# Performance work log

Hardware: AMD Instinct MI355X
Metric: run time of the kernel (lower is better)

## Reference

```python
import jax, jax.numpy as jnp
import numpy as np

DIM = 128
HEADS = 4
DIM_HEAD = 32
HIDDEN = HEADS * DIM_HEAD  # 128
SCALE = DIM_HEAD ** -0.5


def setup_inputs() -> dict:
    key = jax.random.key(0)
    k1, k2, k3, k4 = jax.random.split(key, 4)
    x = jax.random.normal(k1, (2, DIM, 16, 64, 64), dtype=jnp.float32)
    # conv2d 1x1 weights == channel matmuls
    Wqkv = jax.random.normal(k2, (3 * HIDDEN, DIM), dtype=jnp.float32) * (DIM ** -0.5)
    Wout = jax.random.normal(k3, (DIM, HIDDEN), dtype=jnp.float32) * (HIDDEN ** -0.5)
    bout = jax.random.normal(k4, (DIM,), dtype=jnp.float32) * 0.01
    return {"x": x, "Wqkv": Wqkv, "Wout": Wout, "bout": bout}


def reference(x, Wqkv, Wout, bout):
    b, c, f, h, w = x.shape
    n = h * w
    # 'b c f h w -> (b f) c (h w)'
    xf = jnp.transpose(x, (0, 2, 1, 3, 4)).reshape(b * f, c, n)
    # 1x1 conv == channel projection
    qkv = jnp.einsum('oc,bcn->bon', Wqkv, xf)  # (bf, 3*hidden, n)
    q, k, v = jnp.split(qkv, 3, axis=1)
    def to_heads(t):
        return t.reshape(b * f, HEADS, DIM_HEAD, n)  # 'b (h c) n -> b h c n'
    q, k, v = to_heads(q), to_heads(k), to_heads(v)
    q = jax.nn.softmax(q, axis=-2) * SCALE   # softmax over dim_head axis
    k = jax.nn.softmax(k, axis=-1)           # softmax over spatial axis
    v = v / n
    # context: (bf, h, d, e); out: (bf, h, e, n)
    context = jnp.einsum('bhdn,bhen->bhde', k, v)
    out = jnp.einsum('bhde,bhdn->bhen', context, q)
    out = out.reshape(b * f, HIDDEN, n)      # '(h c) merge'
    out = jnp.einsum('oc,bcn->bon', Wout, out) + bout[None, :, None]
    # '(b f) c (h w) -> b c f h w'
    out = out.reshape(b, f, c, h, w).transpose(0, 2, 1, 3, 4)
    return out
```

## Files before the change

### kernel.cpp

```cpp
#include <hip/hip_runtime.h>


constexpr float kSCALE = 0.17677669529663687f;

typedef __attribute__((ext_vector_type(8))) short short8;
typedef __attribute__((ext_vector_type(4))) float f32x4;

__device__ __forceinline__ float bfu2f(unsigned int u) {
  union { unsigned int i; float f; } c; c.i = u << 16; return c.f;
}
__device__ __forceinline__ unsigned short f2bf(float f) {
  union { float f; unsigned int i; } c; c.f = f;
  unsigned int r = c.i + 0x7fffu + ((c.i >> 16) & 1u);
  return (unsigned short)(r >> 16);
}
__device__ __forceinline__ void pack8(const float* v, unsigned short* dst16) {
  union { unsigned short u[8]; uint4 q; } t;
  #pragma unroll
  for (int i = 0; i < 8; ++i) t.u[i] = f2bf(v[i]);
  *(uint4*)dst16 = t.q;
}

__global__ __launch_bounds__(256) void k_wconv(const float* __restrict__ W,
                                               unsigned short* __restrict__ Wbf) {
  const int i = (blockIdx.x * 256 + threadIdx.x) * 4;
  const float4 v = *(const float4*)&W[i];
  union { unsigned short u[4]; uint2 q; } t;
  t.u[0] = f2bf(v.x); t.u[1] = f2bf(v.y); t.u[2] = f2bf(v.z); t.u[3] = f2bf(v.w);
  *(uint2*)&Wbf[i] = t.q;
}

__global__ __launch_bounds__(512, 4) void k_fqkv(const float* __restrict__ x,
                                                 const unsigned short* __restrict__ Wbf,
                                                 unsigned short* __restrict__ qsm,
                                                 float* __restrict__ ctxp,
                                                 float* __restrict__ sexp) {
  __shared__ __align__(16) unsigned short R0[64 * 128];
  __shared__ __align__(16) unsigned short EK[128 * 64];
  __shared__ __align__(16) unsigned short VV[128 * 64];
  const int ntile = blockIdx.x, fr = blockIdx.y;
  const int bb = fr >> 4, ff = fr & 15;
  const int tid = threadIdx.x;
  const float* xfr = x + ((size_t)bb * 2048 + ff) * 4096;

  {
    const int nn = tid & 63, cg = tid >> 6;
    const int ng = ntile * 64 + nn;
    #pragma unroll
    for (int p = 0; p < 2; ++p) {
      const int c8 = cg * 2 + p;
      float v[8];
      #pragma unroll
      for (int j = 0; j < 8; ++j) v[j] = xfr[(size_t)(c8 * 8 + j) * 65536 + ng];
      pack8(v, &R0[nn * 128 + ((c8 * 8) ^ ((nn & 7) << 3))]);
    }
  }
  __syncthreads();

  const int l = tid & 63, w = tid >> 6;
  const int wo = (w >> 1) * 96, wn = (w & 1) * 32;
  const int lr = l & 15, lg = l >> 4;
  f32x4 acc[6][2];
  #pragma unroll
  for (int i = 0; i < 6; ++i) { acc[i][0] = 0.f; acc[i][1] = 0.f; }

  #pragma unroll
  for (int ks = 0; ks < 4; ++ks) {
    const int k0 = ks * 32 + lg * 8;
    short8 a[6], b[2];
    #pragma unroll
    for (int i = 0; i < 6; ++i) a[i] = *(const short8*)&Wbf[(size_t)(wo + 16 * i + lr) * 128 + k0];
    #pragma unroll
    for (int j = 0; j < 2; ++j) {
      const int n = wn + 16 * j + lr;
      b[j] = *(const short8*)&R0[n * 128 + (k0 ^ ((n & 7) << 3))];
    }
    #pragma unroll
    for (int i = 0; i < 6; ++i)
      #pragma unroll
      for (int j = 0; j < 2; ++j)
        acc[i][j] = __builtin_amdgcn_mfma_f32_16x16x32_bf16(a[i], b[j], acc[i][j], 0, 0, 0);
  }

  #pragma unroll
  for (int i = 0; i < 6; ++i) {
    const int grow = wo + 16 * i;
    if (grow >= 128 && grow < 256) {
      #pragma unroll
      for (int j = 0; j < 2; ++j) {
        const int n = wn + 16 * j + lr;
        #pragma unroll
        for (int r = 0; r < 4; ++r) {
          const int dd = grow - 128 + 4 * lg + r;
          EK[dd * 64 + (n ^ ((dd & 7) << 3))] = f2bf(__expf(acc[i][j][r]));
        }
      }
    } else if (grow >= 256) {
      #pragma unroll
      for (int j = 0; j < 2; ++j) {
        const int n = wn + 16 * j + lr;
        #pragma unroll
        for (int r = 0; r < 4; ++r) {
          const int e = grow - 256 + 4 * lg + r;
          VV[e * 64 + (n ^ ((e & 7) << 3))] = f2bf(acc[i][j][r]);
        }
      }
    }
  }
  #pragma unroll
  for (int i0 = 0; i0 < 6; i0 += 2) {
    const int grow0 = wo + 16 * i0;
    if (grow0 < 128) {
      const int h = grow0 >> 5;
      #pragma unroll
      for (int j = 0; j < 2; ++j) {
        const int n = wn + 16 * j + lr;
        float v0[4], v1[4];
        float m = -1e30f;
        #pragma unroll
        for (int r = 0; r < 4; ++r) {
          v0[r] = acc[i0][j][r]; v1[r] = acc[i0 + 1][j][r];
          m = fmaxf(m, fmaxf(v0[r], v1[r]));
        }
        m = fmaxf(m, __shfl_xor(m, 16));
        m = fmaxf(m, __shfl_xor(m, 32));
        float s = 0.f;
        #pragma unroll
        for (int r = 0; r < 4; ++r) {
          v0[r] = __expf(v0[r] - m); v1[r] = __expf(v1[r] - m);
          s += v0[r] + v1[r];
        }
        s += __shfl_xor(s, 16);
        s += __shfl_xor(s, 32);
        const float inv = 1.f / s;
        union { unsigned short u[4]; uint2 q; } t0, t1;
        #pragma unroll
        for (int r = 0; r < 4; ++r) { t0.u[r] = f2bf(v0[r] * inv); t1.u[r] = f2bf(v1[r] * inv); }
        unsigned short* qb = qsm + ((size_t)fr * 4096 + ntile * 64 + n) * 128 + h * 32 + 4 * lg;
        *(uint2*)&qb[0]  = t0.q;
        *(uint2*)&qb[16] = t1.q;
      }
    }
  }
  __syncthreads();

  const int bp = fr * 64 + ntile;
  if (w < 4) {
    const int h = w;
    f32x4 c2[2][2];
    c2[0][0] = 0.f; c2[0][1] = 0.f; c2[1][0] = 0.f; c2[1][1] = 0.f;
    #pragma unroll
    for (int ks = 0; ks < 2; ++ks) {
      const int k0 = ks * 32 + lg * 8;
      short8 a2[2], b2[2];
      #pragma unroll
      for (int i2 = 0; i2 < 2; ++i2) {
        const int row = h * 32 + 16 * i2 + lr;
        a2[i2] = *(const short8*)&EK[row * 64 + (k0 ^ ((row & 7) << 3))];
      }
      #pragma unroll
      for (int j2 = 0; j2 < 2; ++j2) {
        const int row = h * 32 + 16 * j2 + lr;
        b2[j2] = *(const short8*)&VV[row * 64 + (k0 ^ ((row & 7) << 3))];
      }
      #pragma unroll
      for (int i2 = 0; i2 < 2; ++i2)
        #pragma unroll
        for (int j2 = 0; j2 < 2; ++j2)
          c2[i2][j2] = __builtin_amdgcn_mfma_f32_16x16x32_bf16(a2[i2], b2[j2], c2[i2][j2], 0, 0, 0);
    }
    float* cp = ctxp + ((size_t)bp * 4 + h) * 1024;
    #pragma unroll
    for (int i2 = 0; i2 < 2; ++i2)
      #pragma unroll
      for (int j2 = 0; j2 < 2; ++j2)
        #pragma unroll
        for (int r = 0; r < 4; ++r)
          cp[(16 * i2 + 4 * lg + r) * 32 + 16 * j2 + lr] = c2[i2][j2][r];
  } else {
    const int h = w - 4;
    const int rl = l & 31, half = l >> 5;
    const int row = h * 32 + rl;
    float s = 0.f;
    #pragma unroll
    for (int m = 0; m < 4; ++m) {
      const int ng = (half * 32 + m * 8) ^ ((row & 7) << 3);
      const uint4 u = *(const uint4*)&EK[row * 64 + ng];
      s += bfu2f(u.x & 0xffffu) + bfu2f(u.x >> 16) + bfu2f(u.y & 0xffffu) + bfu2f(u.y >> 16)
         + bfu2f(u.z & 0xffffu) + bfu2f(u.z >> 16) + bfu2f(u.w & 0xffffu) + bfu2f(u.w >> 16);
    }
    s += __shfl_xor(s, 32);
    if (half == 0) sexp[(size_t)bp * 128 + row] = s;
  }
}

__global__ __launch_bounds__(256) void k_mbuild(const float* __restrict__ Wout,
                                                const float* __restrict__ ctxp,
                                                const float* __restrict__ sexp,
                                                unsigned short* __restrict__ Mbf) {
  __shared__ float Wo[128][33];
  __shared__ float cn[32][36];
  __shared__ float ses[32];
  const int h = blockIdx.x, fr = blockIdx.y, tid = threadIdx.x;

  float4 c4 = make_float4(0.f, 0.f, 0.f, 0.f);
  {
    const float* base = ctxp + ((size_t)fr * 64) * 4096 + h * 1024 + tid * 4;
    #pragma unroll 8
    for (int p = 0; p < 64; ++p) {
      const float4 v = *(const float4*)&base[(size_t)p * 4096];
      c4.x += v.x; c4.y += v.y; c4.z += v.z; c4.w += v.w;
    }
  }
  if (tid < 32) {
    float s = 0.f;
    const float* sb = sexp + ((size_t)fr * 64) * 128 + h * 32 + tid;
    #pragma unroll 8
    for (int p = 0; p < 64; ++p) s += sb[(size_t)p * 128];
    ses[tid] = s;
  }
  {
    const int o = tid >> 1, e0 = (tid & 1) * 16;
    #pragma unroll
    for (int q = 0; q < 4; ++q) {
      const float4 v = *(const float4*)&Wout[o * 128 + h * 32 + e0 + 4 * q];
      Wo[o][e0 + 4 * q] = v.x; Wo[o][e0 + 4 * q + 1] = v.y;
      Wo[o][e0 + 4 * q + 2] = v.z; Wo[o][e0 + 4 * q + 3] = v.w;
    }
  }
  __syncthreads();
  {
    const int dd = tid >> 3, e0 = (tid & 7) * 4;
    const float sc = kSCALE / (4096.f * ses[dd]);
    cn[dd][e0] = c4.x * sc; cn[dd][e0 + 1] = c4.y * sc;
    cn[dd][e0 + 2] = c4.z * sc; cn[dd][e0 + 3] = c4.w * sc;
  }
  __syncthreads();
  {
    const int o = tid >> 1, dbase = (tid & 1) * 16;
    union { unsigned short u[16]; uint4 q[2]; } t;
    #pragma unroll
    for (int dq = 0; dq < 16; ++dq) {
      const int dc = dbase + dq;
      float s = 0.f;
      #pragma unroll
      for (int e = 0; e < 32; ++e) s = fmaf(Wo[o][e], cn[dc][e], s);
      t.u[dq] = f2bf(s);
    }
    unsigned short* mb = Mbf + (size_t)fr * 16384 + o * 128 + h * 32 + dbase;
    *(uint4*)&mb[0] = t.q[0];
    *(uint4*)&mb[8] = t.q[1];
  }
}

__global__ __launch_bounds__(256, 4) void k_out(const unsigned short* __restrict__ qsm,
                                                const unsigned short* __restrict__ Mbf,
                                                const float* __restrict__ bout,
                                                float* __restrict__ out) {
  __shared__ __align__(16) unsigned short Bp[128 * 128];
  const int ntile = blockIdx.x, fr = blockIdx.y;
  const int bb = fr >> 4, ff = fr & 15;
  const int tid = threadIdx.x;
  {
    const int c8 = (tid & 15) * 8;
    int n = tid >> 4;
    const unsigned short* qb = qsm + ((size_t)fr * 4096 + ntile * 128) * 128;
    #pragma unroll
    for (int p = 0; p < 8; ++p, n += 16) {
      const uint4 qv = *(const uint4*)&qb[n * 128 + c8];
      *(uint4*)&Bp[n * 128 + (c8 ^ ((n & 7) << 3))] = qv;
    }
  }
  __syncthreads();

  const int l = tid & 63, w = tid >> 6;
  const int wo = (w >> 1) * 64, wn = (w & 1) * 64;
  const int lr = l & 15, lg = l >> 4;
  f32x4 acc[4][4];
  #pragma unroll
  for (int i = 0; i < 4; ++i)
    #pragma unroll
    for (int j = 0; j < 4; ++j) acc[i][j] = 0.f;

  const unsigned short* Mf = Mbf + (size_t)fr * 16384;
  #pragma unroll
  for (int ks = 0; ks < 4; ++ks) {
    const int k0 = ks * 32 + lg * 8;
    short8 a[4], b[4];
    #pragma unroll
    for (int i = 0; i < 4; ++i) a[i] = *(const short8*)&Mf[(wo + 16 * i + lr) * 128 + k0];
    #pragma unroll
    for (int j = 0; j < 4; ++j) {
      const int n = wn + 16 * j + lr;
      b[j] = *(const short8*)&Bp[n * 128 + (k0 ^ ((n & 7) << 3))];
    }
    #pragma unroll
    for (int i = 0; i < 4; ++i)
      #pragma unroll
      for (int j = 0; j < 4; ++j)
        acc[i][j] = __builtin_amdgcn_mfma_f32_16x16x32_bf16(a[i], b[j], acc[i][j], 0, 0, 0);
  }

  float* ofr = out + ((size_t)bb * 2048 + ff) * 4096;
  #pragma unroll
  for (int i = 0; i < 4; ++i) {
    const int o0 = wo + 16 * i + 4 * lg;
    const float4 bo = *(const float4*)&bout[o0];
    #pragma unroll
    for (int j = 0; j < 4; ++j) {
      const int n = ntile * 128 + wn + 16 * j + lr;
      ofr[(size_t)(o0 + 0) * 65536 + n] = acc[i][j][0] + bo.x;
      ofr[(size_t)(o0 + 1) * 65536 + n] = acc[i][j][1] + bo.y;
      ofr[(size_t)(o0 + 2) * 65536 + n] = acc[i][j][2] + bo.z;
      ofr[(size_t)(o0 + 3) * 65536 + n] = acc[i][j][3] + bo.w;
    }
  }
}

extern "C" void kernel_launch(void* const* d_in, const int* in_sizes, int n_in,
                              void* d_out, int out_size, void* d_ws, size_t ws_size,
                              hipStream_t stream) {
  const float* x    = (const float*)d_in[0];
  const float* Wqkv = (const float*)d_in[1];
  const float* Wout = (const float*)d_in[2];
  const float* bout = (const float*)d_in[3];
  float* out = (float*)d_out;

  char* ws = (char*)d_ws;
  unsigned short* qsm = (unsigned short*)ws;
  float* ctxp  = (float*)(ws + 33554432u);
  float* sexp  = (float*)(ws + 67108864u);
  unsigned short* Mbf = (unsigned short*)(ws + 68157440u);
  unsigned short* Wbf = (unsigned short*)(ws + 69206016u);

  k_wconv<<<dim3(48), 256, 0, stream>>>(Wqkv, Wbf);
  k_fqkv<<<dim3(64, 32), 512, 0, stream>>>(x, Wbf, qsm, ctxp, sexp);
  k_mbuild<<<dim3(4, 32), 256, 0, stream>>>(Wout, ctxp, sexp, Mbf);
  k_out<<<dim3(32, 32), 256, 0, stream>>>(qsm, Mbf, bout, out);
}
```

Before: 201.1 us.

## Recompute Q projection in output kernel instead of storing softmaxed Q

The first kernel now computes only K and V projections and the context partials. Each block handles 256 spatial positions in four double-buffered sub-tiles, which shrinks the ctxp/sexp partial buffers and the reduction work in k_mbuild. The output kernel re-reads x, recomputes the Q projection and its head-wise softmax in registers, and feeds the result to the second MFMA through lane shuffles. This removes the 32MB bf16 q intermediate write and read, at the cost of reading x twice and doing extra projection math.

```diff
diff --git a/kernel.cpp b/kernel.cpp
--- a/kernel.cpp
+++ b/kernel.cpp
@@ -30,146 +30,129 @@
   *(uint2*)&Wbf[i] = t.q;
 }
 
-__global__ __launch_bounds__(512, 4) void k_fqkv(const float* __restrict__ x,
+__global__ __launch_bounds__(512, 4) void k_ctxp(const float* __restrict__ x,
                                                  const unsigned short* __restrict__ Wbf,
-                                                 unsigned short* __restrict__ qsm,
                                                  float* __restrict__ ctxp,
                                                  float* __restrict__ sexp) {
-  __shared__ __align__(16) unsigned short R0[64 * 128];
+  __shared__ __align__(16) unsigned short R0[2][64 * 128];
   __shared__ __align__(16) unsigned short EK[128 * 64];
   __shared__ __align__(16) unsigned short VV[128 * 64];
-  const int ntile = blockIdx.x, fr = blockIdx.y;
+  const int nt = blockIdx.x, fr = blockIdx.y;
   const int bb = fr >> 4, ff = fr & 15;
   const int tid = threadIdx.x;
   const float* xfr = x + ((size_t)bb * 2048 + ff) * 4096;
-
-  {
-    const int nn = tid & 63, cg = tid >> 6;
-    const int ng = ntile * 64 + nn;
-    #pragma unroll
-    for (int p = 0; p < 2; ++p) {
-      const int c8 = cg * 2 + p;
-      float v[8];
-      #pragma unroll
-      for (int j = 0; j < 8; ++j) v[j] = xfr[(size_t)(c8 * 8 + j) * 65536 + ng];
-      pack8(v, &R0[nn * 128 + ((c8 * 8) ^ ((nn & 7) << 3))]);
-    }
-  }
-  __syncthreads();
+  const int nbase = nt * 256;
 
   const int l = tid & 63, w = tid >> 6;
-  const int wo = (w >> 1) * 96, wn = (w & 1) * 32;
+  const int wo = (w >> 1) * 64, wn = (w & 1) * 32;
   const int lr = l & 15, lg = l >> 4;
-  f32x4 acc[6][2];
-  #pragma unroll
-  for (int i = 0; i < 6; ++i) { acc[i][0] = 0.f; acc[i][1] = 0.f; }
-
-  #pragma unroll
-  for (int ks = 0; ks < 4; ++ks) {
-    const int k0 = ks * 32 + lg * 8;
-    short8 a[6], b[2];
-    #pragma unroll
-    for (int i = 0; i < 6; ++i) a[i] = *(const short8*)&Wbf[(size_t)(wo + 16 * i + lr) * 128 + k0];
-    #pragma unroll
-    for (int j = 0; j < 2; ++j) {
-      const int n = wn + 16 * j + lr;
-      b[j] = *(const short8*)&R0[n * 128 + (k0 ^ ((n & 7) << 3))];
-    }
-    #pragma unroll
-    for (int i = 0; i < 6; ++i)
-      #pragma unroll
-      for (int j = 0; j < 2; ++j)
-        acc[i][j] = __builtin_amdgcn_mfma_f32_16x16x32_bf16(a[i], b[j], acc[i][j], 0, 0, 0);
-  }
-
-  #pragma unroll
-  for (int i = 0; i < 6; ++i) {
-    const int grow = wo + 16 * i;
-    if (grow >= 128 && grow < 256) {
+  const int nn = tid & 63, cg = tid >> 6;
+
+  f32x4 c2[2][2];
+  c2[0][0] = 0.f; c2[0][1] = 0.f; c2[1][0] = 0.f; c2[1][1] = 0.f;
+  float se = 0.f;
+
+  float pre[16];
+  #pragma unroll
+  for (int p = 0; p < 2; ++p)
+    #pragma unroll
+    for (int j = 0; j < 8; ++j)
+      pre[p * 8 + j] = xfr[(size_t)((cg * 2 + p) * 8 + j) * 65536 + nbase + nn];
+
+  #pragma unroll
+  for (int sub = 0; sub < 4; ++sub) {
+    unsigned short* Rb = R0[sub & 1];
+    pack8(pre + 0, &Rb[nn * 128 + ((cg * 16 + 0) ^ ((nn & 7) << 3))]);
+    pack8(pre + 8, &Rb[nn * 128 + ((cg * 16 + 8) ^ ((nn & 7) << 3))]);
+    __syncthreads();
+    if (sub < 3) {
+      #pragma unroll
+      for (int p = 0; p < 2; ++p)
+        #pragma unroll
+        for (int j = 0; j < 8; ++j)
+          pre[p * 8 + j] = xfr[(size_t)((cg * 2 + p) * 8 + j) * 65536 + nbase + (sub + 1) * 64 + nn];
+    }
+    f32x4 acc[4][2];
+    #pragma unroll
+    for (int i = 0; i < 4; ++i) { acc[i][0] = 0.f; acc[i][1] = 0.f; }
+    #pragma unroll
+    for (int ks = 0; ks < 4; ++ks) {
+      const int k0 = ks * 32 + lg * 8;
+      short8 a[4], b[2];
+      #pragma unroll
+      for (int i = 0; i < 4; ++i)
+        a[i] = *(const short8*)&Wbf[(size_t)(128 + wo + 16 * i + lr) * 128 + k0];
       #pragma unroll
       for (int j = 0; j < 2; ++j) {
         const int n = wn + 16 * j + lr;
-        #pragma unroll
-        for (int r = 0; r < 4; ++r) {
-          const int dd = grow - 128 + 4 * lg + r;
-          EK[dd * 64 + (n ^ ((dd & 7) << 3))] = f2bf(__expf(acc[i][j][r]));
+        b[j] = *(const short8*)&Rb[n * 128 + (k0 ^ ((n & 7) << 3))];
+      }
+      #pragma unroll
+      for (int i = 0; i < 4; ++i)
+        #pragma unroll
+        for (int j = 0; j < 2; ++j)
+          acc[i][j] = __builtin_amdgcn_mfma_f32_16x16x32_bf16(a[i], b[j], acc[i][j], 0, 0, 0);
+    }
+    if (wo < 128) {
+      #pragma unroll
+      for (int i = 0; i < 4; ++i)
+        #pragma unroll
+        for (int j = 0; j < 2; ++j) {
+          const int n = wn + 16 * j + lr;
+          #pragma unroll
+          for (int r = 0; r < 4; ++r) {
+            const int dd = wo + 16 * i + 4 * lg + r;
+            EK[dd * 64 + (n ^ ((dd & 7) << 3))] = f2bf(__expf(acc[i][j][r]));
+          }
         }
-      }
-    } else if (grow >= 256) {
-      #pragma unroll
-      for (int j = 0; j < 2; ++j) {
-        const int n = wn + 16 * j + lr;
-        #pragma unroll
-        for (int r = 0; r < 4; ++r) {
-          const int e = grow - 256 + 4 * lg + r;
-          VV[e * 64 + (n ^ ((e & 7) << 3))] = f2bf(acc[i][j][r]);
+    } else {
+      #pragma unroll
+      for (int i = 0; i < 4; ++i)
+        #pragma unroll
+        for (int j = 0; j < 2; ++j) {
+          const int n = wn + 16 * j + lr;
+          #pragma unroll
+          for (int r = 0; r < 4; ++r) {
+            const int e = wo - 128 + 16 * i + 4 * lg + r;
+            VV[e * 64 + (n ^ ((e & 7) << 3))] = f2bf(acc[i][j][r]);
+          }
         }
-      }
-    }
-  }
-  #pragma unroll
-  for (int i0 = 0; i0 < 6; i0 += 2) {
-    const int grow0 = wo + 16 * i0;
-    if (grow0 < 128) {
-      const int h = grow0 >> 5;
-      #pragma unroll
-      for (int j = 0; j < 2; ++j) {
-        const int n = wn + 16 * j + lr;
-        float v0[4], v1[4];
-        float m = -1e30f;
-        #pragma unroll
-        for (int r = 0; r < 4; ++r) {
-          v0[r] = acc[i0][j][r]; v1[r] = acc[i0 + 1][j][r];
-          m = fmaxf(m, fmaxf(v0[r], v1[r]));
+    }
+    __syncthreads();
+    if (w < 4) {
+      const int h = w;
+      #pragma unroll
+      for (int ks2 = 0; ks2 < 2; ++ks2) {
+        const int k0 = ks2 * 32 + lg * 8;
+        short8 a2[2], b2[2];
+        #pragma unroll
+        for (int i2 = 0; i2 < 2; ++i2) {
+          const int row = h * 32 + 16 * i2 + lr;
+          a2[i2] = *(const short8*)&EK[row * 64 + (k0 ^ ((row & 7) << 3))];
+          b2[i2] = *(const short8*)&VV[row * 64 + (k0 ^ ((row & 7) << 3))];
         }
-        m = fmaxf(m, __shfl_xor(m, 16));
-        m = fmaxf(m, __shfl_xor(m, 32));
-        float s = 0.f;
-        #pragma unroll
-        for (int r = 0; r < 4; ++r) {
-          v0[r] = __expf(v0[r] - m); v1[r] = __expf(v1[r] - m);
-          s += v0[r] + v1[r];
-        }
-        s += __shfl_xor(s, 16);
-        s += __shfl_xor(s, 32);
-        const float inv = 1.f / s;
-        union { unsigned short u[4]; uint2 q; } t0, t1;
-        #pragma unroll
-        for (int r = 0; r < 4; ++r) { t0.u[r] = f2bf(v0[r] * inv); t1.u[r] = f2bf(v1[r] * inv); }
-        unsigned short* qb = qsm + ((size_t)fr * 4096 + ntile * 64 + n) * 128 + h * 32 + 4 * lg;
-        *(uint2*)&qb[0]  = t0.q;
-        *(uint2*)&qb[16] = t1.q;
-      }
-    }
-  }
-  __syncthreads();
-
-  const int bp = fr * 64 + ntile;
+        #pragma unroll
+        for (int i2 = 0; i2 < 2; ++i2)
+          #pragma unroll
+          for (int j2 = 0; j2 < 2; ++j2)
+            c2[i2][j2] = __builtin_amdgcn_mfma_f32_16x16x32_bf16(a2[i2], b2[j2], c2[i2][j2], 0, 0, 0);
+      }
+    } else {
+      const int h = w - 4;
+      const int rl = l & 31, half = l >> 5;
+      const int row = h * 32 + rl;
+      #pragma unroll
+      for (int m = 0; m < 4; ++m) {
+        const int ng = (half * 32 + m * 8) ^ ((row & 7) << 3);
+        const uint4 u = *(const uint4*)&EK[row * 64 + ng];
+        se += bfu2f(u.x & 0xffffu) + bfu2f(u.x >> 16) + bfu2f(u.y & 0xffffu) + bfu2f(u.y >> 16)
+            + bfu2f(u.z & 0xffffu) + bfu2f(u.z >> 16) + bfu2f(u.w & 0xffffu) + bfu2f(u.w >> 16);
+      }
+    }
+  }
+  const int bp = fr * 16 + nt;
   if (w < 4) {
-    const int h = w;
-    f32x4 c2[2][2];
-    c2[0][0] = 0.f; c2[0][1] = 0.f; c2[1][0] = 0.f; c2[1][1] = 0.f;
-    #pragma unroll
-    for (int ks = 0; ks < 2; ++ks) {
-      const int k0 = ks * 32 + lg * 8;
-      short8 a2[2], b2[2];
-      #pragma unroll
-      for (int i2 = 0; i2 < 2; ++i2) {
-        const int row = h * 32 + 16 * i2 + lr;
-        a2[i2] = *(const short8*)&EK[row * 64 + (k0 ^ ((row & 7) << 3))];
-      }
-      #pragma unroll
-      for (int j2 = 0; j2 < 2; ++j2) {
-        const int row = h * 32 + 16 * j2 + lr;
-        b2[j2] = *(const short8*)&VV[row * 64 + (k0 ^ ((row & 7) << 3))];
-      }
-      #pragma unroll
-      for (int i2 = 0; i2 < 2; ++i2)
-        #pragma unroll
-        for (int j2 = 0; j2 < 2; ++j2)
-          c2[i2][j2] = __builtin_amdgcn_mfma_f32_16x16x32_bf16(a2[i2], b2[j2], c2[i2][j2], 0, 0, 0);
-    }
-    float* cp = ctxp + ((size_t)bp * 4 + h) * 1024;
+    float* cp = ctxp + ((size_t)bp * 4 + w) * 1024;
     #pragma unroll
     for (int i2 = 0; i2 < 2; ++i2)
       #pragma unroll
@@ -180,17 +163,8 @@
   } else {
     const int h = w - 4;
     const int rl = l & 31, half = l >> 5;
-    const int row = h * 32 + rl;
-    float s = 0.f;
-    #pragma unroll
-    for (int m = 0; m < 4; ++m) {
-      const int ng = (half * 32 + m * 8) ^ ((row & 7) << 3);
-      const uint4 u = *(const uint4*)&EK[row * 64 + ng];
-      s += bfu2f(u.x & 0xffffu) + bfu2f(u.x >> 16) + bfu2f(u.y & 0xffffu) + bfu2f(u.y >> 16)
-         + bfu2f(u.z & 0xffffu) + bfu2f(u.z >> 16) + bfu2f(u.w & 0xffffu) + bfu2f(u.w >> 16);
-    }
-    s += __shfl_xor(s, 32);
-    if (half == 0) sexp[(size_t)bp * 128 + row] = s;
+    se += __shfl_xor(se, 32);
+    if (half == 0) sexp[(size_t)bp * 128 + h * 32 + rl] = se;
   }
 }
 
@@ -205,18 +179,18 @@
 
   float4 c4 = make_float4(0.f, 0.f, 0.f, 0.f);
   {
-    const float* base = ctxp + ((size_t)fr * 64) * 4096 + h * 1024 + tid * 4;
-    #pragma unroll 8
-    for (int p = 0; p < 64; ++p) {
+    const float* base = ctxp + ((size_t)(fr * 16) * 4 + h) * 1024 + tid * 4;
+    #pragma unroll
+    for (int p = 0; p < 16; ++p) {
       const float4 v = *(const float4*)&base[(size_t)p * 4096];
       c4.x += v.x; c4.y += v.y; c4.z += v.z; c4.w += v.w;
     }
   }
   if (tid < 32) {
     float s = 0.f;
-    const float* sb = sexp + ((size_t)fr * 64) * 128 + h * 32 + tid;
-    #pragma unroll 8
-    for (int p = 0; p < 64; ++p) s += sb[(size_t)p * 128];
+    const float* sb = sexp + (size_t)(fr * 16) * 128 + h * 32 + tid;
+    #pragma unroll
+    for (int p = 0; p < 16; ++p) s += sb[(size_t)p * 128];
     ses[tid] = s;
   }
   {
@@ -253,66 +227,135 @@
   }
 }
 
-__global__ __launch_bounds__(256, 4) void k_out(const unsigned short* __restrict__ qsm,
-                                                const unsigned short* __restrict__ Mbf,
-                                                const float* __restrict__ bout,
-                                                float* __restrict__ out) {
-  __shared__ __align__(16) unsigned short Bp[128 * 128];
+__global__ __launch_bounds__(256, 3) void k_fout(const float* __restrict__ x,
+                                                 const unsigned short* __restrict__ Wbf,
+                                                 const unsigned short* __restrict__ Mbf,
+                                                 const float* __restrict__ bout,
+                                                 float* __restrict__ out) {
+  __shared__ __align__(16) unsigned short R0[128 * 128];
   const int ntile = blockIdx.x, fr = blockIdx.y;
   const int bb = fr >> 4, ff = fr & 15;
   const int tid = threadIdx.x;
-  {
-    const int c8 = (tid & 15) * 8;
-    int n = tid >> 4;
-    const unsigned short* qb = qsm + ((size_t)fr * 4096 + ntile * 128) * 128;
-    #pragma unroll
-    for (int p = 0; p < 8; ++p, n += 16) {
-      const uint4 qv = *(const uint4*)&qb[n * 128 + c8];
-      *(uint4*)&Bp[n * 128 + (c8 ^ ((n & 7) << 3))] = qv;
+  const float* xfr = x + ((size_t)bb * 2048 + ff) * 4096;
+
+  {
+    const int nn = tid & 127, cg = tid >> 7;
+    const int ng = ntile * 128 + nn;
+    #pragma unroll
+    for (int p = 0; p < 8; ++p) {
+      const int c8 = cg * 8 + p;
+      float v[8];
+      #pragma unroll
+      for (int j = 0; j < 8; ++j) v[j] = xfr[(size_t)(c8 * 8 + j) * 65536 + ng];
+      pack8(v, &R0[nn * 128 + ((c8 * 8) ^ ((nn & 7) << 3))]);
     }
   }
   __syncthreads();
 
   const int l = tid & 63, w = tid >> 6;
-  const int wo = (w >> 1) * 64, wn = (w & 1) * 64;
+  const int wn = w * 32;
   const int lr = l & 15, lg = l >> 4;
-  f32x4 acc[4][4];
-  #pragma unroll
-  for (int i = 0; i < 4; ++i)
-    #pragma unroll
-    for (int j = 0; j < 4; ++j) acc[i][j] = 0.f;
-
-  const unsigned short* Mf = Mbf + (size_t)fr * 16384;
+
+  f32x4 acc[8][2];
+  #pragma unroll
+  for (int i = 0; i < 8; ++i) { acc[i][0] = 0.f; acc[i][1] = 0.f; }
   #pragma unroll
   for (int ks = 0; ks < 4; ++ks) {
     const int k0 = ks * 32 + lg * 8;
-    short8 a[4], b[4];
-    #pragma unroll
-    for (int i = 0; i < 4; ++i) a[i] = *(const short8*)&Mf[(wo + 16 * i + lr) * 128 + k0];
-    #pragma unroll
-    for (int j = 0; j < 4; ++j) {
+    short8 a[8], b[2];
+    #pragma unroll
+    for (int i = 0; i < 8; ++i) a[i] = *(const short8*)&Wbf[(size_t)(16 * i + lr) * 128 + k0];
+    #pragma unroll
+    for (int j = 0; j < 2; ++j) {
       const int n = wn + 16 * j + lr;
-      b[j] = *(const short8*)&Bp[n * 128 + (k0 ^ ((n & 7) << 3))];
-    }
-    #pragma unroll
-    for (int i = 0; i < 4; ++i)
-      #pragma unroll
-      for (int j = 0; j < 4; ++j)
+      b[j] = *(const short8*)&R0[n * 128 + (k0 ^ ((n & 7) << 3))];
+    }
+    #pragma unroll
+    for (int i = 0; i < 8; ++i)
+      #pragma unroll
+      for (int j = 0; j < 2; ++j)
         acc[i][j] = __builtin_amdgcn_mfma_f32_16x16x32_bf16(a[i], b[j], acc[i][j], 0, 0, 0);
   }
 
+  #pragma unroll
+  for (int h = 0; h < 4; ++h) {
+    #pragma unroll
+    for (int j = 0; j < 2; ++j) {
+      float m = -1e30f;
+      #pragma unroll
+      for (int r = 0; r < 4; ++r) m = fmaxf(m, fmaxf(acc[2 * h][j][r], acc[2 * h + 1][j][r]));
+      m = fmaxf(m, __shfl_xor(m, 16));
+      m = fmaxf(m, __shfl_xor(m, 32));
+      float e0[4], e1[4], s = 0.f;
+      #pragma unroll
+      for (int r = 0; r < 4; ++r) {
+        e0[r] = __expf(acc[2 * h][j][r] - m);
+        e1[r] = __expf(acc[2 * h + 1][j][r] - m);
+        s += e0[r] + e1[r];
+      }
+      s += __shfl_xor(s, 16);
+      s += __shfl_xor(s, 32);
+      const float inv = 1.f / s;
+      #pragma unroll
+      for (int r = 0; r < 4; ++r) {
+        acc[2 * h][j][r] = e0[r] * inv;
+        acc[2 * h + 1][j][r] = e1[r] * inv;
+      }
+    }
+  }
+  unsigned int pk[8][2][2];
+  #pragma unroll
+  for (int i = 0; i < 8; ++i)
+    #pragma unroll
+    for (int j = 0; j < 2; ++j) {
+      pk[i][j][0] = (unsigned int)f2bf(acc[i][j][0]) | ((unsigned int)f2bf(acc[i][j][1]) << 16);
+      pk[i][j][1] = (unsigned int)f2bf(acc[i][j][2]) | ((unsigned int)f2bf(acc[i][j][3]) << 16);
+    }
+
+  const int src0 = lr + ((lg & 1) ? 32 : 0);
+  const int src1 = src0 + 16;
+  const bool hi = (lg & 2) != 0;
+  f32x4 acc2[8][2];
+  #pragma unroll
+  for (int i = 0; i < 8; ++i) { acc2[i][0] = 0.f; acc2[i][1] = 0.f; }
+  const unsigned short* Mf = Mbf + (size_t)fr * 16384;
+  #pragma unroll
+  for (int ks = 0; ks < 4; ++ks) {
+    const int k0 = ks * 32 + lg * 8;
+    short8 a2[8];
+    #pragma unroll
+    for (int i2 = 0; i2 < 8; ++i2) a2[i2] = *(const short8*)&Mf[(16 * i2 + lr) * 128 + k0];
+    short8 b[2];
+    #pragma unroll
+    for (int j = 0; j < 2; ++j) {
+      const unsigned int s0 = hi ? pk[2 * ks + 1][j][0] : pk[2 * ks][j][0];
+      const unsigned int s1 = hi ? pk[2 * ks + 1][j][1] : pk[2 * ks][j][1];
+      union { int u[4]; short8 s8; } t;
+      t.u[0] = __shfl((int)s0, src0);
+      t.u[1] = __shfl((int)s1, src0);
+      t.u[2] = __shfl((int)s0, src1);
+      t.u[3] = __shfl((int)s1, src1);
+      b[j] = t.s8;
+    }
+    #pragma unroll
+    for (int i2 = 0; i2 < 8; ++i2)
+      #pragma unroll
+      for (int j = 0; j < 2; ++j)
+        acc2[i2][j] = __builtin_amdgcn_mfma_f32_16x16x32_bf16(a2[i2], b[j], acc2[i2][j], 0, 0, 0);
+  }
+
   float* ofr = out + ((size_t)bb * 2048 + ff) * 4096;
   #pragma unroll
-  for (int i = 0; i < 4; ++i) {
-    const int o0 = wo + 16 * i + 4 * lg;
+  for (int i2 = 0; i2 < 8; ++i2) {
+    const int o0 = 16 * i2 + 4 * lg;
     const float4 bo = *(const float4*)&bout[o0];
     #pragma unroll
-    for (int j = 0; j < 4; ++j) {
+    for (int j = 0; j < 2; ++j) {
       const int n = ntile * 128 + wn + 16 * j + lr;
-      ofr[(size_t)(o0 + 0) * 65536 + n] = acc[i][j][0] + bo.x;
-      ofr[(size_t)(o0 + 1) * 65536 + n] = acc[i][j][1] + bo.y;
-      ofr[(size_t)(o0 + 2) * 65536 + n] = acc[i][j][2] + bo.z;
-      ofr[(size_t)(o0 + 3) * 65536 + n] = acc[i][j][3] + bo.w;
+      ofr[(size_t)(o0 + 0) * 65536 + n] = acc2[i2][j][0] + bo.x;
+      ofr[(size_t)(o0 + 1) * 65536 + n] = acc2[i2][j][1] + bo.y;
+      ofr[(size_t)(o0 + 2) * 65536 + n] = acc2[i2][j][2] + bo.z;
+      ofr[(size_t)(o0 + 3) * 65536 + n] = acc2[i2][j][3] + bo.w;
     }
   }
 }
@@ -327,14 +370,13 @@
   float* out = (float*)d_out;
 
   char* ws = (char*)d_ws;
-  unsigned short* qsm = (unsigned short*)ws;
-  float* ctxp  = (float*)(ws + 33554432u);
-  float* sexp  = (float*)(ws + 67108864u);
-  unsigned short* Mbf = (unsigned short*)(ws + 68157440u);
-  unsigned short* Wbf = (unsigned short*)(ws + 69206016u);
+  float* ctxp = (float*)ws;
+  float* sexp = (float*)(ws + 8388608u);
+  unsigned short* Mbf = (unsigned short*)(ws + 8650752u);
+  unsigned short* Wbf = (unsigned short*)(ws + 9699328u);
 
   k_wconv<<<dim3(48), 256, 0, stream>>>(Wqkv, Wbf);
-  k_fqkv<<<dim3(64, 32), 512, 0, stream>>>(x, Wbf, qsm, ctxp, sexp);
+  k_ctxp<<<dim3(16, 32), 512, 0, stream>>>(x, Wbf, ctxp, sexp);
   k_mbuild<<<dim3(4, 32), 256, 0, stream>>>(Wout, ctxp, sexp, Mbf);
-  k_out<<<dim3(32, 32), 256, 0, stream>>>(qsm, Mbf, bout, out);
-}
+  k_fout<<<dim3(32, 32), 256, 0, stream>>>(x, Wbf, Mbf, bout, out);
+}
```

Measured after the change: 242.5 us. +20.6%, slower.
